# Kernel tuning notes

Measured on AMD Instinct MI355X. Metric: run time of the kernel, lower is better.

## Reference

```python
import jax, jax.numpy as jnp
import numpy as np

NM = 50000   # member nodes
NP = 50000   # provider nodes
DM = 96      # member feature dim
DP = 128     # provider feature dim
IN_DIM = 128
HID = 256
LAT = 64
E = 1000000


def _sage_conv(x, src, dst, n, Wl, Wr, b):
    # PyG SAGEConv, mean aggregation: out = lin_l(mean_j x_j) + lin_r(x)
    msg = x[src]                                           # [E2, F]
    agg = jax.ops.segment_sum(msg, dst, num_segments=n)    # [N, F]
    deg = jax.ops.segment_sum(jnp.ones(src.shape[0], x.dtype), dst, num_segments=n)
    agg = agg / jnp.maximum(deg, 1.0)[:, None]
    return agg @ Wl.T + b + x @ Wr.T


def setup_inputs() -> dict:
    key = jax.random.key(0)
    ks = jax.random.split(key, 12)
    def g(k, shape, scale):
        return jax.random.normal(k, shape, jnp.float32) * scale
    inp = {
        "x_member": jax.random.normal(ks[0], (NM, DM), jnp.float32),
        "x_provider": jax.random.normal(ks[1], (NP, DP), jnp.float32),
        "edge_index": jnp.stack([
            jax.random.randint(ks[2], (E,), 0, NP),   # provider idx
            jax.random.randint(ks[3], (E,), 0, NM),   # member idx
        ], axis=0),
        # SAGEConv 1
        "W1l": g(ks[4], (HID, IN_DIM), (1.0 / IN_DIM) ** 0.5),
        "W1r": g(ks[5], (HID, IN_DIM), (1.0 / IN_DIM) ** 0.5),
        "b1": jnp.zeros((HID,), jnp.float32),
        # SAGEConv 2
        "W2l": g(ks[6], (LAT, HID), (1.0 / HID) ** 0.5),
        "W2r": g(ks[7], (LAT, HID), (1.0 / HID) ** 0.5),
        "b2": jnp.zeros((LAT,), jnp.float32),
        # decoder Linear(latent, in_dim)
        "Wd": g(ks[8], (IN_DIM, LAT), (1.0 / LAT) ** 0.5),
        "bd": jnp.zeros((IN_DIM,), jnp.float32),
    }
    return inp


def reference(x_member, x_provider, edge_index, W1l, W1r, b1, W2l, W2r, b2, Wd, bd):
    # pad member features to max_dim and concat (members first)
    xm = jnp.pad(x_member, ((0, 0), (0, IN_DIM - DM)))
    x = jnp.concatenate([xm, x_provider], axis=0)          # [NM+NP, IN_DIM]

    provider_idx = edge_index[0]
    member_idx = edge_index[1]
    # faithful to source: member indices are offset by NM in the combined graph
    src = jnp.concatenate([provider_idx, member_idx + NM])
    dst = jnp.concatenate([member_idx + NM, provider_idx])
    n = NM + NP

    h = jax.nn.relu(_sage_conv(x, src, dst, n, W1l, W1r, b1))
    # dropout: eval mode -> identity
    z = _sage_conv(h, src, dst, n, W2l, W2r, b2)            # [N, LAT]
    x_hat = z @ Wd.T + bd                                   # [N, IN_DIM]

    x_hat_member = x_hat[:NM]
    x_hat_provider = x_hat[NM:]
    member_z = z[:NM]
    provider_z = z[NM:]
    edge_logits = jnp.sum(provider_z[provider_idx] * member_z[member_idx], axis=1)
    return (x_hat_member, x_hat_provider, edge_logits)
```

## Files before the change

### kernel.cpp

```cpp
#include <hip/hip_runtime.h>
#include <stdint.h>

#define NMEM 50000
#define NTOT 100000
#define DMEM 96
#define DPRV 128
#define IND  128
#define HID  256
#define LATD 64
#define NEDGE 1000000

#define NB   196
#define VSH  9
#define NBV  512
#define EPB  4096

typedef __bf16 v8bf  __attribute__((ext_vector_type(8)));
typedef float  f32x4 __attribute__((ext_vector_type(4)));

__device__ __forceinline__ float bf2f(uint32_t u) {
    union { uint32_t u; float f; } x; x.u = u << 16; return x.f;
}
__device__ __forceinline__ uint32_t f2bf(float f) {
    union { float f; uint32_t u; } x; x.f = f;
    uint32_t r = x.u + 0x7fffu + ((x.u >> 16) & 1u);
    return r >> 16;
}
__device__ __forceinline__ int ld_ei(const int* ei, int idx, int i64) {
    return i64 ? ei[2 * idx] : ei[idx];
}

__global__ void k_detect(const uint16_t* __restrict__ w1l, const int* __restrict__ ei,
                         int* __restrict__ flags) {
    __shared__ int c1, c2;
    if (threadIdx.x == 0) { c1 = 0; c2 = 0; }
    __syncthreads();
    int big = 0;
    for (int i = threadIdx.x; i < 32768; i += 256) {
        float w = bf2f(w1l[i]);
        if (!(w > -2.0f && w < 2.0f)) big++;
    }
    int zhi = 0;
    for (int j = threadIdx.x; j < 2048; j += 256)
        if (ei[2 * j + 1] == 0) zhi++;
    atomicAdd(&c1, big);
    atomicAdd(&c2, zhi);
    __syncthreads();
    if (threadIdx.x == 0) {
        flags[0] = (c1 > 64) ? 1 : 0;
        flags[1] = (c2 > 1024) ? 1 : 0;
    }
}

__global__ void k_canon(const void* w1l, const void* w1r, const void* w2l,
                        const void* w2r, const void* wd, const void* b1,
                        const void* b2, const void* bd,
                        uint16_t* __restrict__ dstw, float* __restrict__ dstb,
                        const int* __restrict__ flags) {
    int g = blockIdx.x * 256 + threadIdx.x;
    int f32in = flags[0];
    if (g < 106496) {
        const void* src; int off;
        if (g < 65536) { int n = g >> 8, k = g & 255;
            src = (k < 128) ? w1l : w1r; off = n * 128 + (k & 127); }
        else if (g < 81920) { src = w2l; off = g - 65536; }
        else if (g < 98304) { src = w2r; off = g - 81920; }
        else                { src = wd;  off = g - 98304; }
        dstw[g] = f32in ? (uint16_t)f2bf(((const float*)src)[off])
                        : ((const uint16_t*)src)[off];
    } else if (g < 106944) {
        int o = g - 106496;
        const void* src; int off;
        if (o < 256)      { src = b1; off = o; }
        else if (o < 320) { src = b2; off = o - 256; }
        else              { src = bd; off = o - 320; }
        dstb[o] = f32in ? ((const float*)src)[off] : bf2f(((const uint16_t*)src)[off]);
    }
}

__global__ void k_build_x(const void* xm, const void* xp, uint16_t* __restrict__ Px,
                          uint16_t* __restrict__ Rx, const int* __restrict__ flags) {
    int idx = blockIdx.x * 256 + threadIdx.x;
    if (idx >= NTOT * 16) return;
    int v = idx >> 4, dblk = idx & 15;
    int d0 = dblk * 8;
    int f32in = flags[0];
    union { uint4 q; uint16_t u[8]; } o;
    if (v < NMEM) {
        if (d0 < DMEM) {
            if (f32in) {
                const float* s = (const float*)xm + (size_t)v * DMEM + d0;
                uint4 lo = *(const uint4*)s;
                uint4 hi = *(const uint4*)(s + 4);
                const float* lf = (const float*)&lo;
                const float* hf = (const float*)&hi;
#pragma unroll
                for (int i = 0; i < 4; i++) o.u[i] = (uint16_t)f2bf(lf[i]);
#pragma unroll
                for (int i = 0; i < 4; i++) o.u[4 + i] = (uint16_t)f2bf(hf[i]);
            } else {
                o.q = *(const uint4*)((const uint16_t*)xm + (size_t)v * DMEM + d0);
            }
        } else {
            o.q = (uint4){0, 0, 0, 0};
        }
    } else {
        int vv = v - NMEM;
        if (f32in) {
            const float* s = (const float*)xp + (size_t)vv * DPRV + d0;
            uint4 lo = *(const uint4*)s;
            uint4 hi = *(const uint4*)(s + 4);
            const float* lf = (const float*)&lo;
            const float* hf = (const float*)&hi;
#pragma unroll
            for (int i = 0; i < 4; i++) o.u[i] = (uint16_t)f2bf(lf[i]);
#pragma unroll
            for (int i = 0; i < 4; i++) o.u[4 + i] = (uint16_t)f2bf(hf[i]);
        } else {
            o.q = *(const uint4*)((const uint16_t*)xp + (size_t)vv * DPRV + d0);
        }
    }
    if (d0 < 64) *(uint4*)(Px + (size_t)v * 64 + d0) = o.q;
    else         *(uint4*)(Rx + (size_t)v * 64 + (d0 - 64)) = o.q;
}

__global__ __launch_bounds__(256) void k_pcount(const int* __restrict__ ei,
                                                int* __restrict__ bcount,
                                                const int* __restrict__ flags) {
    __shared__ int h[NB];
    int t = threadIdx.x;
    for (int i = t; i < NB; i += 256) h[i] = 0;
    __syncthreads();
    int i64 = flags[1];
    int j0 = blockIdx.x * EPB;
    int jend = min(j0 + EPB, NEDGE);
    for (int j = j0 + t; j < jend; j += 256) {
        int p = ld_ei(ei, j, i64), m = ld_ei(ei, NEDGE + j, i64);
        atomicAdd(&h[(NMEM + m) >> VSH], 1);
        atomicAdd(&h[p >> VSH], 1);
    }
    __syncthreads();
    for (int i = t; i < NB; i += 256) atomicAdd(&bcount[i], h[i]);
}

__global__ void k_bscan(const int* __restrict__ bcount, int* __restrict__ bbase,
                        int* __restrict__ bcursor, int* __restrict__ row_start) {
    __shared__ int s[256];
    int t = threadIdx.x;
    int v = (t < NB) ? bcount[t] : 0;
    s[t] = v; __syncthreads();
    for (int off = 1; off < 256; off <<= 1) {
        int x = (t >= off) ? s[t - off] : 0;
        __syncthreads();
        s[t] += x;
        __syncthreads();
    }
    if (t < NB) { bbase[t] = s[t] - v; bcursor[t] = s[t] - v; }
    if (t == 0) { bbase[NB] = 2 * NEDGE; row_start[NTOT] = 2 * NEDGE; }
}

__global__ __launch_bounds__(256) void k_part(const int* __restrict__ ei,
                                              int* __restrict__ bcursor,
                                              uint32_t* __restrict__ part,
                                              const int* __restrict__ flags) {
    __shared__ int h[NB], gb[NB], cur[NB];
    int t = threadIdx.x;
    for (int i = t; i < NB; i += 256) { h[i] = 0; cur[i] = 0; }
    __syncthreads();
    int i64 = flags[1];
    int j0 = blockIdx.x * EPB;
    int jend = min(j0 + EPB, NEDGE);
    for (int j = j0 + t; j < jend; j += 256) {
        int p = ld_ei(ei, j, i64), m = ld_ei(ei, NEDGE + j, i64);
        atomicAdd(&h[(NMEM + m) >> VSH], 1);
        atomicAdd(&h[p >> VSH], 1);
    }
    __syncthreads();
    for (int i = t; i < NB; i += 256) gb[i] = atomicAdd(&bcursor[i], h[i]);
    __syncthreads();
    for (int j = j0 + t; j < jend; j += 256) {
        int p = ld_ei(ei, j, i64), m = ld_ei(ei, NEDGE + j, i64);
        int d1 = NMEM + m;
        int d2 = p;
        int b1 = d1 >> VSH, b2 = d2 >> VSH;
        int r1 = atomicAdd(&cur[b1], 1);
        part[gb[b1] + r1] = ((uint32_t)(d1 & (NBV - 1)) << 17) | (uint32_t)p;
        int r2 = atomicAdd(&cur[b2], 1);
        part[gb[b2] + r2] = ((uint32_t)(d2 & (NBV - 1)) << 17) | (uint32_t)(NMEM + m);
    }
}

__global__ __launch_bounds__(256) void k_sort(const uint32_t* __restrict__ part,
                                              const int* __restrict__ bbase,
                                              int* __restrict__ row_start,
                                              int* __restrict__ colg) {
    __shared__ int sa[NBV], sb[NBV];
    int k = blockIdx.x, t = threadIdx.x;
    int base = bbase[k];
    int cnt  = bbase[k + 1] - base;
    for (int i = t; i < NBV; i += 256) sa[i] = 0;
    __syncthreads();
    for (int i = t; i < cnt; i += 256) {
        uint32_t e = part[base + i];
        atomicAdd(&sa[e >> 17], 1);
    }
    __syncthreads();
    int* src = sa; int* dst = sb;
    for (int off = 1; off < NBV; off <<= 1) {
        for (int i = t; i < NBV; i += 256)
            dst[i] = src[i] + (i >= off ? src[i - off] : 0);
        __syncthreads();
        int* tmp = src; src = dst; dst = tmp;
    }
    for (int i = t; i < NBV; i += 256) {
        int excl = (i > 0) ? src[i - 1] : 0;
        dst[i] = excl;
        int gv = (k << VSH) + i;
        if (gv < NTOT) row_start[gv] = base + excl;
    }
    __syncthreads();
    for (int i = t; i < cnt; i += 256) {
        uint32_t e = part[base + i];
        int dloc = (int)(e >> 17);
        int pos = atomicAdd(&dst[dloc], 1);
        colg[base + pos] = (int)(e & 0x1FFFFu);
    }
}

__global__ __launch_bounds__(256) void k_agg1(const uint16_t* __restrict__ Px,
                                              const uint16_t* __restrict__ Rx,
                                              const int* __restrict__ row_start,
                                              const int* __restrict__ colg,
                                              uint16_t* __restrict__ A1) {
    int t = threadIdx.x;
    int half = (t & 63) >> 5;
    int v = blockIdx.x * 8 + (t >> 6) * 2 + half;
    int l32 = t & 31;
    int slot = l32 >> 4, cg = l32 & 15;
    const uint16_t* base = (cg < 8) ? Px : Rx;
    int co = (cg & 7) * 8;
    int start = row_start[v], end = row_start[v + 1];
    float a0[8] = {0.f, 0.f, 0.f, 0.f, 0.f, 0.f, 0.f, 0.f};
    float a1[8] = {0.f, 0.f, 0.f, 0.f, 0.f, 0.f, 0.f, 0.f};
    int b = start + slot;
    for (; b + 2 < end; b += 4) {
        int s0 = colg[b], s1 = colg[b + 2];
        union { uint4 q; uint16_t u[8]; } f0, f1;
        f0.q = *(const uint4*)(base + (size_t)s0 * 64 + co);
        f1.q = *(const uint4*)(base + (size_t)s1 * 64 + co);
#pragma unroll
        for (int i = 0; i < 8; i++) { a0[i] += bf2f(f0.u[i]); a1[i] += bf2f(f1.u[i]); }
    }
    if (b < end) {
        int s0 = colg[b];
        union { uint4 q; uint16_t u[8]; } f0;
        f0.q = *(const uint4*)(base + (size_t)s0 * 64 + co);
#pragma unroll
        for (int i = 0; i < 8; i++) a0[i] += bf2f(f0.u[i]);
    }
#pragma unroll
    for (int i = 0; i < 8; i++) {
        a0[i] += a1[i];
        a0[i] += __shfl_xor(a0[i], 16);
    }
    if (slot == 0) {
        float inv = 1.0f / (float)max(end - start, 1);
        union { uint4 q; uint16_t u[8]; } o;
#pragma unroll
        for (int i = 0; i < 8; i++) o.u[i] = (uint16_t)f2bf(a0[i] * inv);
        *(uint4*)(A1 + (size_t)v * 128 + cg * 8) = o.q;
    }
}

__global__ __launch_bounds__(256, 2) void k_gemm1(const uint16_t* __restrict__ A1,
                                                  const uint16_t* __restrict__ canonb,
                                                  const float* __restrict__ biasf,
                                                  uint16_t* __restrict__ P,
                                                  uint16_t* __restrict__ R) {
    __shared__ uint16_t As[128][264];
    int t = threadIdx.x;
    int w = t >> 6, lane = t & 63;
    int m16 = lane & 15, q = lane >> 4;
    int row0 = blockIdx.x * 128;

    uint4 stg[16];
#pragma unroll
    for (int i = 0; i < 16; i++) {
        int c = t + i * 256;
        int row = c >> 5, seg = c & 31;
        int grow = min(row0 + row, NTOT - 1);
        int k0 = seg * 8;
        const uint16_t* src;
        if (k0 < 128)      src = A1 + (size_t)grow * 128 + k0;
        else if (k0 < 192) src = P + (size_t)grow * 64 + (k0 - 128);
        else               src = R + (size_t)grow * 64 + (k0 - 192);
        stg[i] = *(const uint4*)src;
    }
#pragma unroll
    for (int i = 0; i < 16; i++) {
        int c = t + i * 256;
        int row = c >> 5, seg = c & 31;
        *(uint4*)&As[row][seg * 8] = stg[i];
    }
    __syncthreads();

    uint32_t hpk[4][8][2];
#pragma unroll
    for (int p = 0; p < 2; p++) {
        v8bf b1[2][8];
#pragma unroll
        for (int n = 0; n < 2; n++) {
            int col = w * 64 + (p * 2 + n) * 16 + m16;
#pragma unroll
            for (int ks = 0; ks < 8; ks++)
                b1[n][ks] = *(const v8bf*)(canonb + (size_t)col * 256 + ks * 32 + q * 8);
        }
        f32x4 acc[8][2];
#pragma unroll
        for (int mt = 0; mt < 8; mt++) {
            acc[mt][0] = (f32x4){0.f, 0.f, 0.f, 0.f};
            acc[mt][1] = (f32x4){0.f, 0.f, 0.f, 0.f};
        }
#pragma unroll
        for (int mt = 0; mt < 8; mt++) {
#pragma unroll
            for (int ks = 0; ks < 8; ks++) {
                v8bf a = *(const v8bf*)&As[mt * 16 + m16][ks * 32 + q * 8];
                acc[mt][0] = __builtin_amdgcn_mfma_f32_16x16x32_bf16(b1[0][ks], a, acc[mt][0], 0, 0, 0);
                acc[mt][1] = __builtin_amdgcn_mfma_f32_16x16x32_bf16(b1[1][ks], a, acc[mt][1], 0, 0, 0);
            }
        }
#pragma unroll
        for (int n = 0; n < 2; n++) {
            int cb = w * 64 + (p * 2 + n) * 16 + q * 4;
            f32x4 bb = *(const f32x4*)&biasf[cb];
#pragma unroll
            for (int mt = 0; mt < 8; mt++) {
                float v0 = fmaxf(acc[mt][n][0] + bb[0], 0.f);
                float v1 = fmaxf(acc[mt][n][1] + bb[1], 0.f);
                float v2 = fmaxf(acc[mt][n][2] + bb[2], 0.f);
                float v3 = fmaxf(acc[mt][n][3] + bb[3], 0.f);
                hpk[p * 2 + n][mt][0] = f2bf(v0) | (f2bf(v1) << 16);
                hpk[p * 2 + n][mt][1] = f2bf(v2) | (f2bf(v3) << 16);
            }
        }
        if (p == 0) __builtin_amdgcn_sched_barrier(0);
    }
    __syncthreads();

#pragma unroll
    for (int pn = 0; pn < 4; pn++) {
        int cb = w * 64 + pn * 16 + q * 4;
#pragma unroll
        for (int mt = 0; mt < 8; mt++) {
            uint2 v; v.x = hpk[pn][mt][0]; v.y = hpk[pn][mt][1];
            *(uint2*)&As[mt * 16 + m16][cb] = v;
        }
    }
    __syncthreads();

    v8bf b2[2][8];
#pragma unroll
    for (int n = 0; n < 2; n++) {
        int c2 = w * 32 + n * 16 + m16;
        const uint16_t* s2 = canonb + (c2 < 64 ? (65536 + c2 * 256) : (81920 + (c2 - 64) * 256));
#pragma unroll
        for (int ks = 0; ks < 8; ks++)
            b2[n][ks] = *(const v8bf*)(s2 + ks * 32 + q * 8);
    }
    f32x4 acc2[8][2];
#pragma unroll
    for (int mt = 0; mt < 8; mt++) {
        acc2[mt][0] = (f32x4){0.f, 0.f, 0.f, 0.f};
        acc2[mt][1] = (f32x4){0.f, 0.f, 0.f, 0.f};
    }
#pragma unroll
    for (int mt = 0; mt < 8; mt++) {
#pragma unroll
        for (int ks = 0; ks < 8; ks++) {
            v8bf hf = *(const v8bf*)&As[mt * 16 + m16][ks * 32 + q * 8];
            acc2[mt][0] = __builtin_amdgcn_mfma_f32_16x16x32_bf16(b2[0][ks], hf, acc2[mt][0], 0, 0, 0);
            acc2[mt][1] = __builtin_amdgcn_mfma_f32_16x16x32_bf16(b2[1][ks], hf, acc2[mt][1], 0, 0, 0);
        }
    }
#pragma unroll
    for (int n = 0; n < 2; n++) {
        int cb = w * 32 + n * 16 + q * 4;
        int isR = cb >= 64;
        int cl = cb - (isR ? 64 : 0);
        f32x4 bb;
        if (isR) bb = *(const f32x4*)&biasf[256 + cl];
        else     bb = (f32x4){0.f, 0.f, 0.f, 0.f};
        uint16_t* dst = isR ? R : P;
#pragma unroll
        for (int mt = 0; mt < 8; mt++) {
            int row = row0 + mt * 16 + m16;
            if (row < NTOT) {
                uint2 v;
                v.x = f2bf(acc2[mt][n][0] + bb[0]) | (f2bf(acc2[mt][n][1] + bb[1]) << 16);
                v.y = f2bf(acc2[mt][n][2] + bb[2]) | (f2bf(acc2[mt][n][3] + bb[3]) << 16);
                *(uint2*)(dst + (size_t)row * 64 + cl) = v;
            }
        }
    }
}

__global__ __launch_bounds__(256) void k_agg2z(const uint16_t* __restrict__ P,
                                               const uint16_t* __restrict__ R,
                                               const int* __restrict__ row_start,
                                               const int* __restrict__ colg,
                                               uint16_t* __restrict__ Z) {
    int t = threadIdx.x;
    int half = (t & 63) >> 5;
    int v = blockIdx.x * 8 + (t >> 6) * 2 + half;
    int l32 = t & 31;
    int slot = l32 >> 3, cg = l32 & 7;
    int start = row_start[v], end = row_start[v + 1];
    float a0[8] = {0.f, 0.f, 0.f, 0.f, 0.f, 0.f, 0.f, 0.f};
    float a1[8] = {0.f, 0.f, 0.f, 0.f, 0.f, 0.f, 0.f, 0.f};
    int b = start + slot;
    for (; b + 4 < end; b += 8) {
        int s0 = colg[b], s1 = colg[b + 4];
        union { uint4 q; uint16_t u[8]; } f0, f1;
        f0.q = *(const uint4*)(P + (size_t)s0 * 64 + cg * 8);
        f1.q = *(const uint4*)(P + (size_t)s1 * 64 + cg * 8);
#pragma unroll
        for (int i = 0; i < 8; i++) { a0[i] += bf2f(f0.u[i]); a1[i] += bf2f(f1.u[i]); }
    }
    if (b < end) {
        int s0 = colg[b];
        union { uint4 q; uint16_t u[8]; } f0;
        f0.q = *(const uint4*)(P + (size_t)s0 * 64 + cg * 8);
#pragma unroll
        for (int i = 0; i < 8; i++) a0[i] += bf2f(f0.u[i]);
    }
#pragma unroll
    for (int i = 0; i < 8; i++) {
        a0[i] += a1[i];
        a0[i] += __shfl_xor(a0[i], 8);
        a0[i] += __shfl_xor(a0[i], 16);
    }
    if (slot == 0) {
        float inv = 1.0f / (float)max(end - start, 1);
        union { uint4 q; uint16_t u[8]; } rr, o;
        rr.q = *(const uint4*)(R + (size_t)v * 64 + cg * 8);
#pragma unroll
        for (int i = 0; i < 8; i++)
            o.u[i] = (uint16_t)f2bf(a0[i] * inv + bf2f(rr.u[i]));
        *(uint4*)(Z + (size_t)v * 64 + cg * 8) = o.q;
    }
}

__global__ __launch_bounds__(256, 2) void k_gemm3(const uint16_t* __restrict__ Z,
                                                  const uint16_t* __restrict__ canonb,
                                                  const float* __restrict__ biasf,
                                                  float* __restrict__ outf) {
    int wave = threadIdx.x >> 6, lane = threadIdx.x & 63;
    int m16 = lane & 15, quad = lane >> 4;
    int row0 = (blockIdx.x * 4 + wave) * 16;
    int arow = min(row0 + m16, NTOT - 1);
    v8bf a0 = *(const v8bf*)(Z + (size_t)arow * 64 + quad * 8);
    v8bf a1 = *(const v8bf*)(Z + (size_t)arow * 64 + 32 + quad * 8);
    v8bf b0[8], b1[8];
#pragma unroll
    for (int nt = 0; nt < 8; nt++) {
        b0[nt] = *(const v8bf*)(canonb + 98304 + (size_t)(nt * 16 + m16) * 64 + quad * 8);
        b1[nt] = *(const v8bf*)(canonb + 98304 + (size_t)(nt * 16 + m16) * 64 + 32 + quad * 8);
    }
    f32x4 acc[8];
#pragma unroll
    for (int i = 0; i < 8; i++) acc[i] = (f32x4){0.f, 0.f, 0.f, 0.f};
#pragma unroll
    for (int nt = 0; nt < 8; nt++) {
        acc[nt] = __builtin_amdgcn_mfma_f32_16x16x32_bf16(a0, b0[nt], acc[nt], 0, 0, 0);
        acc[nt] = __builtin_amdgcn_mfma_f32_16x16x32_bf16(a1, b1[nt], acc[nt], 0, 0, 0);
    }
#pragma unroll
    for (int nt = 0; nt < 8; nt++) {
        int col = nt * 16 + m16;
        float bia = biasf[320 + col];
#pragma unroll
        for (int r = 0; r < 4; r++) {
            int row = row0 + quad * 4 + r;
            if (row < NTOT) outf[(size_t)row * 128 + col] = acc[nt][r] + bia;
        }
    }
}

__global__ __launch_bounds__(256) void k_logits(const int* __restrict__ ei,
                                                const uint16_t* __restrict__ Z,
                                                float* __restrict__ out,
                                                const int* __restrict__ flags) {
    int t = blockIdx.x * 256 + threadIdx.x;
    int j = t >> 3, sub = t & 7;
    if (j >= NEDGE) return;
    int i64 = flags[1];
    int p = ld_ei(ei, j, i64), m = ld_ei(ei, NEDGE + j, i64);
    union { uint4 q; uint16_t u[8]; } a, b;
    a.q = *(const uint4*)(Z + (size_t)(NMEM + p) * 64 + sub * 8);
    b.q = *(const uint4*)(Z + (size_t)m * 64 + sub * 8);
    float d = 0.f;
#pragma unroll
    for (int i = 0; i < 8; i++) d += bf2f(a.u[i]) * bf2f(b.u[i]);
    d += __shfl_xor(d, 1);
    d += __shfl_xor(d, 2);
    d += __shfl_xor(d, 4);
    if (sub == 0) out[j] = d;
}

__global__ void k_zero_out(float* __restrict__ out, int n4) {
    int i = blockIdx.x * 256 + threadIdx.x;
    if (i < n4) ((uint4*)out)[i] = (uint4){0, 0, 0, 0};
}
__global__ void k_sentinel(float* __restrict__ out, const int* __restrict__ flags,
                           int ws_mb) {
    if (blockIdx.x == 0 && threadIdx.x == 0)
        out[0] = 1000.0f + (float)ws_mb + 4096.0f * flags[0] + 8192.0f * flags[1];
}

extern "C" void kernel_launch(void* const* d_in, const int* in_sizes, int n_in,
                              void* d_out, int out_size, void* d_ws, size_t ws_size,
                              hipStream_t stream) {
    const void* xm = d_in[0];
    const void* xp = d_in[1];
    const int*  ei = (const int*)d_in[2];
    float* outf = (float*)d_out;

    const size_t NEED = 73019648;
    if (ws_size < NEED) {
        int* flags = (int*)d_ws;
        k_detect<<<1, 256, 0, stream>>>((const uint16_t*)d_in[3], ei, flags);
        int n4 = out_size / 4;
        k_zero_out<<<(n4 + 255) / 256, 256, 0, stream>>>(outf, n4);
        k_sentinel<<<1, 64, 0, stream>>>(outf, flags, (int)(ws_size >> 20));
        return;
    }

    char* ws = (char*)d_ws;
    int* colg       = (int*)(ws + 0);
    int* bmeta      = (int*)(ws + 8000000);
    int* bucket_count  = bmeta;
    int* bucket_base   = bmeta + 256;
    int* bucket_cursor = bmeta + 512;
    int* row_start  = (int*)(ws + 8400384);
    int* flags      = (int*)(ws + 8800768) + 100;
    uint16_t* canonb= (uint16_t*)(ws + 8804864);
    float* biasf    = (float*)(ws + 9017856);
    uint16_t* A1    = (uint16_t*)(ws + 9019648);
    uint32_t* part  = (uint32_t*)A1;
    uint16_t* P     = (uint16_t*)(ws + 34619648);
    uint16_t* R     = (uint16_t*)(ws + 47419648);
    uint16_t* Z     = (uint16_t*)(ws + 60219648);

    const int PGRID = (NEDGE + EPB - 1) / EPB;

    k_detect<<<1, 256, 0, stream>>>((const uint16_t*)d_in[3], ei, flags);
    k_canon<<<418, 256, 0, stream>>>(d_in[3], d_in[4], d_in[6], d_in[7], d_in[9],
                                     d_in[5], d_in[8], d_in[10], canonb, biasf, flags);
    k_build_x<<<(NTOT * 16 + 255) / 256, 256, 0, stream>>>(xm, xp, P, R, flags);
    hipMemsetAsync(bucket_count, 0, 256 * sizeof(int), stream);
    k_pcount<<<PGRID, 256, 0, stream>>>(ei, bucket_count, flags);
    k_bscan<<<1, 256, 0, stream>>>(bucket_count, bucket_base, bucket_cursor, row_start);
    k_part<<<PGRID, 256, 0, stream>>>(ei, bucket_cursor, part, flags);
    k_sort<<<NB, 256, 0, stream>>>(part, bucket_base, row_start, colg);
    k_agg1<<<NTOT / 8, 256, 0, stream>>>(P, R, row_start, colg, A1);
    k_gemm1<<<782, 256, 0, stream>>>(A1, canonb, biasf, P, R);
    k_agg2z<<<NTOT / 8, 256, 0, stream>>>(P, R, row_start, colg, Z);
    k_gemm3<<<1563, 256, 0, stream>>>(Z, canonb, biasf, outf);
    k_logits<<<NEDGE * 8 / 256, 256, 0, stream>>>(ei, Z, outf + 12800000, flags);
}
```

Baseline: 394.6 us.

## Halve gemm1 row tile, raise occupancy, and unroll agg1 gather loop deeper

The fused two-layer GEMM kernel now handles 64 rows per block instead of 128. That halves shared memory and accumulator registers so launch bounds can request 4 blocks per SM, and it restructures the first-layer loop to one 16-column tile at a time. The first aggregation kernel keeps four independent gathers in flight instead of two, to hide more memory latency. The costs are reloading weight fragments across twice as many blocks and a small increase in tail-loop overhead.

```diff
diff --git a/kernel.cpp b/kernel.cpp
--- a/kernel.cpp
+++ b/kernel.cpp
@@ -242,16 +242,23 @@
     int start = row_start[v], end = row_start[v + 1];
     float a0[8] = {0.f, 0.f, 0.f, 0.f, 0.f, 0.f, 0.f, 0.f};
     float a1[8] = {0.f, 0.f, 0.f, 0.f, 0.f, 0.f, 0.f, 0.f};
+    float a2[8] = {0.f, 0.f, 0.f, 0.f, 0.f, 0.f, 0.f, 0.f};
+    float a3[8] = {0.f, 0.f, 0.f, 0.f, 0.f, 0.f, 0.f, 0.f};
     int b = start + slot;
-    for (; b + 2 < end; b += 4) {
-        int s0 = colg[b], s1 = colg[b + 2];
-        union { uint4 q; uint16_t u[8]; } f0, f1;
+    for (; b + 6 < end; b += 8) {
+        int s0 = colg[b], s1 = colg[b + 2], s2 = colg[b + 4], s3 = colg[b + 6];
+        union { uint4 q; uint16_t u[8]; } f0, f1, f2, f3;
         f0.q = *(const uint4*)(base + (size_t)s0 * 64 + co);
         f1.q = *(const uint4*)(base + (size_t)s1 * 64 + co);
-#pragma unroll
-        for (int i = 0; i < 8; i++) { a0[i] += bf2f(f0.u[i]); a1[i] += bf2f(f1.u[i]); }
-    }
-    if (b < end) {
+        f2.q = *(const uint4*)(base + (size_t)s2 * 64 + co);
+        f3.q = *(const uint4*)(base + (size_t)s3 * 64 + co);
+#pragma unroll
+        for (int i = 0; i < 8; i++) {
+            a0[i] += bf2f(f0.u[i]); a1[i] += bf2f(f1.u[i]);
+            a2[i] += bf2f(f2.u[i]); a3[i] += bf2f(f3.u[i]);
+        }
+    }
+    for (; b < end; b += 2) {
         int s0 = colg[b];
         union { uint4 q; uint16_t u[8]; } f0;
         f0.q = *(const uint4*)(base + (size_t)s0 * 64 + co);
@@ -260,7 +267,7 @@
     }
 #pragma unroll
     for (int i = 0; i < 8; i++) {
-        a0[i] += a1[i];
+        a0[i] += a1[i] + a2[i] + a3[i];
         a0[i] += __shfl_xor(a0[i], 16);
     }
     if (slot == 0) {
@@ -272,20 +279,20 @@
     }
 }
 
-__global__ __launch_bounds__(256, 2) void k_gemm1(const uint16_t* __restrict__ A1,
+__global__ __launch_bounds__(256, 4) void k_gemm1(const uint16_t* __restrict__ A1,
                                                   const uint16_t* __restrict__ canonb,
                                                   const float* __restrict__ biasf,
                                                   uint16_t* __restrict__ P,
                                                   uint16_t* __restrict__ R) {
-    __shared__ uint16_t As[128][264];
+    __shared__ uint16_t As[64][264];
     int t = threadIdx.x;
     int w = t >> 6, lane = t & 63;
     int m16 = lane & 15, q = lane >> 4;
-    int row0 = blockIdx.x * 128;
-
-    uint4 stg[16];
-#pragma unroll
-    for (int i = 0; i < 16; i++) {
+    int row0 = blockIdx.x * 64;
+
+    uint4 stg[8];
+#pragma unroll
+    for (int i = 0; i < 8; i++) {
         int c = t + i * 256;
         int row = c >> 5, seg = c & 31;
         int grow = min(row0 + row, NTOT - 1);
@@ -297,54 +304,43 @@
         stg[i] = *(const uint4*)src;
     }
 #pragma unroll
-    for (int i = 0; i < 16; i++) {
+    for (int i = 0; i < 8; i++) {
         int c = t + i * 256;
-        int row = c >> 5, seg = c & 31;
-        *(uint4*)&As[row][seg * 8] = stg[i];
-    }
-    __syncthreads();
-
-    uint32_t hpk[4][8][2];
-#pragma unroll
-    for (int p = 0; p < 2; p++) {
-        v8bf b1[2][8];
-#pragma unroll
-        for (int n = 0; n < 2; n++) {
-            int col = w * 64 + (p * 2 + n) * 16 + m16;
-#pragma unroll
-            for (int ks = 0; ks < 8; ks++)
-                b1[n][ks] = *(const v8bf*)(canonb + (size_t)col * 256 + ks * 32 + q * 8);
-        }
-        f32x4 acc[8][2];
-#pragma unroll
-        for (int mt = 0; mt < 8; mt++) {
-            acc[mt][0] = (f32x4){0.f, 0.f, 0.f, 0.f};
-            acc[mt][1] = (f32x4){0.f, 0.f, 0.f, 0.f};
-        }
-#pragma unroll
-        for (int mt = 0; mt < 8; mt++) {
+        *(uint4*)&As[c >> 5][(c & 31) * 8] = stg[i];
+    }
+    __syncthreads();
+
+    uint32_t hpk[4][4][2];
+#pragma unroll
+    for (int pn = 0; pn < 4; pn++) {
+        int col = w * 64 + pn * 16 + m16;
+        v8bf b1[8];
+#pragma unroll
+        for (int ks = 0; ks < 8; ks++)
+            b1[ks] = *(const v8bf*)(canonb + (size_t)col * 256 + ks * 32 + q * 8);
+        f32x4 acc[4];
+#pragma unroll
+        for (int mt = 0; mt < 4; mt++) acc[mt] = (f32x4){0.f, 0.f, 0.f, 0.f};
+#pragma unroll
+        for (int mt = 0; mt < 4; mt++) {
 #pragma unroll
             for (int ks = 0; ks < 8; ks++) {
                 v8bf a = *(const v8bf*)&As[mt * 16 + m16][ks * 32 + q * 8];
-                acc[mt][0] = __builtin_amdgcn_mfma_f32_16x16x32_bf16(b1[0][ks], a, acc[mt][0], 0, 0, 0);
-                acc[mt][1] = __builtin_amdgcn_mfma_f32_16x16x32_bf16(b1[1][ks], a, acc[mt][1], 0, 0, 0);
+                acc[mt] = __builtin_amdgcn_mfma_f32_16x16x32_bf16(b1[ks], a, acc[mt], 0, 0, 0);
             }
         }
-#pragma unroll
-        for (int n = 0; n < 2; n++) {
-            int cb = w * 64 + (p * 2 + n) * 16 + q * 4;
-            f32x4 bb = *(const f32x4*)&biasf[cb];
-#pragma unroll
-            for (int mt = 0; mt < 8; mt++) {
-                float v0 = fmaxf(acc[mt][n][0] + bb[0], 0.f);
-                float v1 = fmaxf(acc[mt][n][1] + bb[1], 0.f);
-                float v2 = fmaxf(acc[mt][n][2] + bb[2], 0.f);
-                float v3 = fmaxf(acc[mt][n][3] + bb[3], 0.f);
-                hpk[p * 2 + n][mt][0] = f2bf(v0) | (f2bf(v1) << 16);
-                hpk[p * 2 + n][mt][1] = f2bf(v2) | (f2bf(v3) << 16);
-            }
-        }
-        if (p == 0) __builtin_amdgcn_sched_barrier(0);
+        int cb = w * 64 + pn * 16 + q * 4;
+        f32x4 bb = *(const f32x4*)&biasf[cb];
+#pragma unroll
+        for (int mt = 0; mt < 4; mt++) {
+            float v0 = fmaxf(acc[mt][0] + bb[0], 0.f);
+            float v1 = fmaxf(acc[mt][1] + bb[1], 0.f);
+            float v2 = fmaxf(acc[mt][2] + bb[2], 0.f);
+            float v3 = fmaxf(acc[mt][3] + bb[3], 0.f);
+            hpk[pn][mt][0] = f2bf(v0) | (f2bf(v1) << 16);
+            hpk[pn][mt][1] = f2bf(v2) | (f2bf(v3) << 16);
+        }
+        __builtin_amdgcn_sched_barrier(0);
     }
     __syncthreads();
 
@@ -352,7 +348,7 @@
     for (int pn = 0; pn < 4; pn++) {
         int cb = w * 64 + pn * 16 + q * 4;
 #pragma unroll
-        for (int mt = 0; mt < 8; mt++) {
+        for (int mt = 0; mt < 4; mt++) {
             uint2 v; v.x = hpk[pn][mt][0]; v.y = hpk[pn][mt][1];
             *(uint2*)&As[mt * 16 + m16][cb] = v;
         }
@@ -368,14 +364,14 @@
         for (int ks = 0; ks < 8; ks++)
             b2[n][ks] = *(const v8bf*)(s2 + ks * 32 + q * 8);
     }
-    f32x4 acc2[8][2];
-#pragma unroll
-    for (int mt = 0; mt < 8; mt++) {
+    f32x4 acc2[4][2];
+#pragma unroll
+    for (int mt = 0; mt < 4; mt++) {
         acc2[mt][0] = (f32x4){0.f, 0.f, 0.f, 0.f};
         acc2[mt][1] = (f32x4){0.f, 0.f, 0.f, 0.f};
     }
 #pragma unroll
-    for (int mt = 0; mt < 8; mt++) {
+    for (int mt = 0; mt < 4; mt++) {
 #pragma unroll
         for (int ks = 0; ks < 8; ks++) {
             v8bf hf = *(const v8bf*)&As[mt * 16 + m16][ks * 32 + q * 8];
@@ -393,7 +389,7 @@
         else     bb = (f32x4){0.f, 0.f, 0.f, 0.f};
         uint16_t* dst = isR ? R : P;
 #pragma unroll
-        for (int mt = 0; mt < 8; mt++) {
+        for (int mt = 0; mt < 4; mt++) {
             int row = row0 + mt * 16 + m16;
             if (row < NTOT) {
                 uint2 v;
@@ -564,7 +560,7 @@
     k_part<<<PGRID, 256, 0, stream>>>(ei, bucket_cursor, part, flags);
     k_sort<<<NB, 256, 0, stream>>>(part, bucket_base, row_start, colg);
     k_agg1<<<NTOT / 8, 256, 0, stream>>>(P, R, row_start, colg, A1);
-    k_gemm1<<<782, 256, 0, stream>>>(A1, canonb, biasf, P, R);
+    k_gemm1<<<(NTOT + 63) / 64, 256, 0, stream>>>(A1, canonb, biasf, P, R);
     k_agg2z<<<NTOT / 8, 256, 0, stream>>>(P, R, row_start, colg, Z);
     k_gemm3<<<1563, 256, 0, stream>>>(Z, canonb, biasf, outf);
     k_logits<<<NEDGE * 8 / 256, 256, 0, stream>>>(ei, Z, outf + 12800000, flags);
```

Measured after the change: 400.0 us. Within noise of the previous version (+1.4%).
